# Performance work log

Hardware: AMD Instinct MI355X
Metric: run time of the kernel (lower is better)

## Reference

```python
import jax, jax.numpy as jnp
import numpy as np

D_MODEL, D_FF, D_KEY, D_VALUE, NUM_HEADS = 1024, 4096, 64, 64, 16
EPS = 1e-5
B, S = 2, 2048


def layer_norm(x, gamma, beta):
    # torch x.var() default is unbiased (ddof=1)
    mean = jnp.mean(x, axis=-1, keepdims=True)
    var = jnp.var(x, axis=-1, keepdims=True, ddof=1)
    return (x - mean) / jnp.sqrt(var + EPS) * gamma + beta


def setup_inputs() -> dict:
    key = jax.random.key(0)
    ks = jax.random.split(key, 16)
    s = 0.02
    return {
        "x": jax.random.normal(ks[0], (B, S, D_MODEL), dtype=jnp.float32),
        "mask": jnp.zeros((B, 1, 1, S), dtype=bool),
        "Wq": jax.random.normal(ks[1], (D_MODEL, NUM_HEADS * D_KEY), dtype=jnp.float32) * s,
        "bq": jnp.zeros((NUM_HEADS * D_KEY,), jnp.float32),
        "Wk": jax.random.normal(ks[2], (D_MODEL, NUM_HEADS * D_KEY), dtype=jnp.float32) * s,
        "bk": jnp.zeros((NUM_HEADS * D_KEY,), jnp.float32),
        "Wv": jax.random.normal(ks[3], (D_MODEL, NUM_HEADS * D_VALUE), dtype=jnp.float32) * s,
        "bv": jnp.zeros((NUM_HEADS * D_VALUE,), jnp.float32),
        "Wo": jax.random.normal(ks[4], (NUM_HEADS * D_VALUE, D_MODEL), dtype=jnp.float32) * s,
        "bo": jnp.zeros((D_MODEL,), jnp.float32),
        "gamma1": jnp.ones((D_MODEL,), jnp.float32),
        "beta1": jnp.zeros((D_MODEL,), jnp.float32),
        "W1": jax.random.normal(ks[5], (D_MODEL, D_FF), dtype=jnp.float32) * s,
        "b1": jnp.zeros((D_FF,), jnp.float32),
        "W2": jax.random.normal(ks[6], (D_FF, D_MODEL), dtype=jnp.float32) * s,
        "b2": jnp.zeros((D_MODEL,), jnp.float32),
        "gamma2": jnp.ones((D_MODEL,), jnp.float32),
        "beta2": jnp.zeros((D_MODEL,), jnp.float32),
    }


def reference(x, mask, Wq, bq, Wk, bk, Wv, bv, Wo, bo, gamma1, beta1, W1, b1, W2, b2, gamma2, beta2):
    Bsz, Sq, _ = x.shape
    # ---- multi-head attention (self-attention) ----
    q = (x @ Wq + bq).reshape(Bsz, Sq, NUM_HEADS, D_KEY)
    k = (x @ Wk + bk).reshape(Bsz, Sq, NUM_HEADS, D_KEY)
    v = (x @ Wv + bv).reshape(Bsz, Sq, NUM_HEADS, D_VALUE)
    scores = jnp.einsum("bqhd,bkhd->bhqk", q, k) / jnp.sqrt(jnp.float32(D_KEY))
    scores = jnp.where(mask, -jnp.inf, scores)
    attn = jax.nn.softmax(scores, axis=-1)
    ctx = jnp.einsum("bhqk,bkhd->bqhd", attn, v).reshape(Bsz, Sq, NUM_HEADS * D_VALUE)
    attn_out = ctx @ Wo + bo
    # ---- residual + LN, FFN, residual + LN ----
    h = layer_norm(attn_out + x, gamma1, beta1)
    ff = jnp.maximum(h @ W1 + b1, 0.0) @ W2 + b2
    out = layer_norm(ff + h, gamma2, beta2)
    return out
```

## Files before the change

kernel.cpp:

```cpp
#include <hip/hip_runtime.h>
#include <cstddef>
#include <cstdint>

#define BATCH   2
#define SEQ     2048
#define DMODEL  1024
#define DFF     4096
#define NHEADS  16
#define DHEAD   64
#define NTOK    (BATCH * SEQ)
#define LN_EPS  1e-5f

typedef __attribute__((ext_vector_type(8))) short bf16x8;
typedef __attribute__((ext_vector_type(4))) float f32x4;

#define MFMA(a, b, c) __builtin_amdgcn_mfma_f32_16x16x32_bf16((a), (b), (c), 0, 0, 0)

__device__ __forceinline__ unsigned short f2bf(float f) {
    unsigned int u = __float_as_uint(f);
    u += 0x7fffu + ((u >> 16) & 1u);
    return (unsigned short)(u >> 16);
}

__device__ __forceinline__ void gld_lds16(const void* g, void* l) {
    __builtin_amdgcn_global_load_lds(
        (const __attribute__((address_space(1))) void*)g,
        (__attribute__((address_space(3))) void*)l, 16, 0, 0);
}

template <int NT, bool RELU, bool RES, bool OUTBF16>
__global__ __launch_bounds__(256) void gemm_bt(
    const short* __restrict__ A, const short* __restrict__ Bt,
    const float* __restrict__ bias, const float* __restrict__ res,
    void* __restrict__ Cout, int M, int N, int K)
{
    constexpr int MI = (NT == 128) ? 4 : 2;
    __shared__ __align__(16) short As[128][32];
    __shared__ __align__(16) short Bs[NT][32];

    const int tid  = threadIdx.x;
    const int lane = tid & 63;
    const int w    = tid >> 6;
    const int row0 = blockIdx.y * 128;
    const int col0 = blockIdx.x * NT;
    const int wr   = (NT == 128) ? (w >> 1) * 64 : w * 32;
    const int wc   = (NT == 128) ? (w & 1) * 64 : 0;
    const int m    = lane & 15;
    const int q    = lane >> 4;

    f32x4 acc[MI][4] = {};

    const int sra = w * 32;
    const short* ga = A + (size_t)(row0 + sra + (lane >> 2)) * K + (lane & 3) * 8;
    short* lA0 = &As[sra][0];
    short* lA1 = &As[sra + 16][0];
    const int srb = (NT == 128) ? w * 32 : w * 16;
    const short* gb = Bt + (size_t)(col0 + srb + (lane >> 2)) * K + (lane & 3) * 8;
    short* lB0 = &Bs[srb][0];
    short* lB1 = (NT == 128) ? &Bs[srb + 16][0] : nullptr;

    for (int k0 = 0; k0 < K; k0 += 32) {
        gld_lds16(ga + k0, lA0);
        gld_lds16(ga + (size_t)16 * K + k0, lA1);
        gld_lds16(gb + k0, lB0);
        if (NT == 128) gld_lds16(gb + (size_t)16 * K + k0, lB1);
        __syncthreads();

        bf16x8 af[MI], bfr[4];
#pragma unroll
        for (int i = 0; i < MI; ++i) af[i]  = *(const bf16x8*)&As[wr + i * 16 + m][q * 8];
#pragma unroll
        for (int i = 0; i < 4; ++i)  bfr[i] = *(const bf16x8*)&Bs[wc + i * 16 + m][q * 8];
#pragma unroll
        for (int mi = 0; mi < MI; ++mi)
#pragma unroll
            for (int ni = 0; ni < 4; ++ni)
                acc[mi][ni] = MFMA(af[mi], bfr[ni], acc[mi][ni]);
        __syncthreads();
    }

#pragma unroll
    for (int mi = 0; mi < MI; ++mi) {
#pragma unroll
        for (int ni = 0; ni < 4; ++ni) {
            const int col = col0 + wc + ni * 16 + m;
            const float bv = bias[col];
#pragma unroll
            for (int r = 0; r < 4; ++r) {
                const int row = row0 + wr + mi * 16 + q * 4 + r;
                float v = acc[mi][ni][r] + bv;
                if (RES)  v += res[(size_t)row * N + col];
                if (RELU) v = fmaxf(v, 0.0f);
                if (OUTBF16)
                    ((unsigned short*)Cout)[(size_t)row * N + col] = f2bf(v);
                else
                    ((float*)Cout)[(size_t)row * N + col] = v;
            }
        }
    }
}

__global__ __launch_bounds__(256) void gemm_qkv(
    const short* __restrict__ A, const short* __restrict__ Bt,
    const float* __restrict__ bias, short* __restrict__ QKb,
    unsigned short* __restrict__ Vt)
{
    const int K = DMODEL;
    __shared__ __align__(16) short As[128][32];
    __shared__ __align__(16) short Bs[128][32];

    const int tid  = threadIdx.x;
    const int lane = tid & 63;
    const int w    = tid >> 6;
    const int row0 = blockIdx.y * 128;
    const int col0 = blockIdx.x * 128;
    const int wr   = (w >> 1) * 64;
    const int wc   = (w & 1) * 64;
    const int m    = lane & 15;
    const int q    = lane >> 4;

    f32x4 acc[4][4] = {};

    const int sr = w * 32;
    const short* ga = A  + (size_t)(row0 + sr + (lane >> 2)) * K + (lane & 3) * 8;
    const short* gb = Bt + (size_t)(col0 + sr + (lane >> 2)) * K + (lane & 3) * 8;
    short* lA0 = &As[sr][0];
    short* lA1 = &As[sr + 16][0];
    short* lB0 = &Bs[sr][0];
    short* lB1 = &Bs[sr + 16][0];

    for (int k0 = 0; k0 < K; k0 += 32) {
        gld_lds16(ga + k0, lA0);
        gld_lds16(ga + (size_t)16 * K + k0, lA1);
        gld_lds16(gb + k0, lB0);
        gld_lds16(gb + (size_t)16 * K + k0, lB1);
        __syncthreads();
        bf16x8 af[4], bfr[4];
#pragma unroll
        for (int i = 0; i < 4; ++i) af[i]  = *(const bf16x8*)&As[wr + i * 16 + m][q * 8];
#pragma unroll
        for (int i = 0; i < 4; ++i) bfr[i] = *(const bf16x8*)&Bs[wc + i * 16 + m][q * 8];
#pragma unroll
        for (int mi = 0; mi < 4; ++mi)
#pragma unroll
            for (int ni = 0; ni < 4; ++ni)
                acc[mi][ni] = MFMA(af[mi], bfr[ni], acc[mi][ni]);
        __syncthreads();
    }

    const int mode = (col0 >= 2048) ? 2 : (col0 < 1024 ? 0 : 1);
    const float scale = (mode == 0) ? 0.125f : 1.0f;
#pragma unroll
    for (int mi = 0; mi < 4; ++mi) {
#pragma unroll
        for (int ni = 0; ni < 4; ++ni) {
            const int col = col0 + wc + ni * 16 + m;
            const float bv = bias[col];
#pragma unroll
            for (int r = 0; r < 4; ++r) {
                const int row = row0 + wr + mi * 16 + q * 4 + r;
                const float v = (acc[mi][ni][r] + bv) * scale;
                if (mode < 2) {
                    QKb[(size_t)row * 2048 + col] = (short)f2bf(v);
                } else {
                    const int hd  = col - 2048;
                    const int bb  = row >> 11;
                    const int key = row & (SEQ - 1);
                    Vt[((size_t)(bb * 1024 + hd)) * SEQ + key] = f2bf(v);
                }
            }
        }
    }
}

__global__ __launch_bounds__(256) void attn_mfma(
    const short* __restrict__ Qp,
    const short* __restrict__ Kp,
    const short* __restrict__ Vtg,
    unsigned short* __restrict__ CTX)
{
    __shared__ __align__(16) short Ks[2][64][64];
    __shared__ __align__(16) short Vs[2][64][64];
    __shared__ __align__(16) short Ps[4][16][64];

    const int tid  = threadIdx.x;
    const int lane = tid & 63;
    const int w    = tid >> 6;
    const int b    = blockIdx.z;
    const int h    = blockIdx.y;
    const int q0   = blockIdx.x * 64;
    const int m    = lane & 15;
    const int qd   = lane >> 4;

    const short* gq = Qp + (size_t)(b * SEQ + q0 + w * 16 + m) * 2048 + h * 64;
    bf16x8 qreg[2];
    qreg[0] = *(const bf16x8*)(gq + qd * 8);
    qreg[1] = *(const bf16x8*)(gq + (qd + 4) * 8);

    const int cg = (lane & 7) ^ (lane >> 3);
    const short* Kg = Kp  + (size_t)(b * SEQ) * 2048 + h * 64 + cg * 8;
    const short* Vg = Vtg + (size_t)(b * 1024 + h * 64) * SEQ + cg * 8;

    {
        const short* gk = Kg + (size_t)(w * 16 + (lane >> 3)) * 2048;
        gld_lds16(gk,            &Ks[0][w * 16][0]);
        gld_lds16(gk + 8 * 2048, &Ks[0][w * 16 + 8][0]);
        const short* gv = Vg + (size_t)(w * 16 + (lane >> 3)) * SEQ;
        gld_lds16(gv,            &Vs[0][w * 16][0]);
        gld_lds16(gv + 8 * SEQ,  &Vs[0][w * 16 + 8][0]);
    }

    float lrow[4] = {0.f, 0.f, 0.f, 0.f};
    f32x4 oacc[4] = {};

    for (int j = 0; j < SEQ / 64; ++j) {
        const int cur = j & 1;
        __syncthreads();
        if (j + 1 < SEQ / 64) {
            const int nb = 1 - cur;
            const short* gk = Kg + (size_t)((j + 1) * 64 + w * 16 + (lane >> 3)) * 2048;
            gld_lds16(gk,            &Ks[nb][w * 16][0]);
            gld_lds16(gk + 8 * 2048, &Ks[nb][w * 16 + 8][0]);
            const short* gv = Vg + (size_t)(w * 16 + (lane >> 3)) * SEQ + (j + 1) * 64;
            gld_lds16(gv,            &Vs[nb][w * 16][0]);
            gld_lds16(gv + 8 * SEQ,  &Vs[nb][w * 16 + 8][0]);
        }

        f32x4 sacc[4] = {};
#pragma unroll
        for (int ks = 0; ks < 2; ++ks) {
            const int kc = ks * 4 + qd;
#pragma unroll
            for (int ni = 0; ni < 4; ++ni) {
                const int kn = ni * 16 + m;
                bf16x8 bk = *(const bf16x8*)&Ks[cur][kn][(kc ^ (kn & 7)) * 8];
                sacc[ni] = MFMA(qreg[ks], bk, sacc[ni]);
            }
        }

        float rsum[4] = {0.f, 0.f, 0.f, 0.f};
#pragma unroll
        for (int ni = 0; ni < 4; ++ni)
#pragma unroll
            for (int r = 0; r < 4; ++r) {
                const float p = __expf(sacc[ni][r]);
                sacc[ni][r] = p;
                rsum[r] += p;
            }
#pragma unroll
        for (int off = 1; off < 16; off <<= 1)
#pragma unroll
            for (int r = 0; r < 4; ++r) rsum[r] += __shfl_xor(rsum[r], off, 64);
#pragma unroll
        for (int r = 0; r < 4; ++r) lrow[r] += rsum[r];

#pragma unroll
        for (int ni = 0; ni < 4; ++ni)
#pragma unroll
            for (int r = 0; r < 4; ++r) {
                const int row = qd * 4 + r;
                const int swc = (ni * 2 + (m >> 3)) ^ (row & 7);
                Ps[w][row][swc * 8 + (m & 7)] = (short)f2bf(sacc[ni][r]);
            }

#pragma unroll
        for (int ks = 0; ks < 2; ++ks) {
            const int kc = ks * 4 + qd;
            bf16x8 ap = *(const bf16x8*)&Ps[w][m][(kc ^ (m & 7)) * 8];
#pragma unroll
            for (int ni = 0; ni < 4; ++ni) {
                const int dn = ni * 16 + m;
                bf16x8 bv = *(const bf16x8*)&Vs[cur][dn][(kc ^ (dn & 7)) * 8];
                oacc[ni] = MFMA(ap, bv, oacc[ni]);
            }
        }
    }

    float inv[4];
#pragma unroll
    for (int r = 0; r < 4; ++r) inv[r] = 1.0f / lrow[r];
#pragma unroll
    for (int ni = 0; ni < 4; ++ni)
#pragma unroll
        for (int r = 0; r < 4; ++r) {
            const int row = q0 + w * 16 + qd * 4 + r;
            const int col = h * 64 + ni * 16 + m;
            CTX[(size_t)(b * SEQ + row) * DMODEL + col] = f2bf(oacc[ni][r] * inv[r]);
        }
}

__global__ __launch_bounds__(256) void wtrans(
    const float* __restrict__ W, short* __restrict__ Wt, int K, int N)
{
    __shared__ float t[32][33];
    const int tid = threadIdx.x;
    const int c = tid & 31, r8 = tid >> 5;
    const int bx = blockIdx.x * 32, by = blockIdx.y * 32;
#pragma unroll
    for (int i = 0; i < 4; ++i)
        t[r8 + i * 8][c] = W[(size_t)(by + r8 + i * 8) * N + bx + c];
    __syncthreads();
#pragma unroll
    for (int i = 0; i < 4; ++i)
        Wt[(size_t)(bx + r8 + i * 8) * K + by + c] = (short)f2bf(t[c][r8 + i * 8]);
}

__global__ __launch_bounds__(256) void xconv(
    const float* __restrict__ X, short* __restrict__ Y)
{
    const size_t i = ((size_t)blockIdx.x * 256 + threadIdx.x) * 4;
    const float4 v = *(const float4*)(X + i);
    short4 o;
    o.x = (short)f2bf(v.x); o.y = (short)f2bf(v.y);
    o.z = (short)f2bf(v.z); o.w = (short)f2bf(v.w);
    *(short4*)(Y + i) = o;
}

__global__ __launch_bounds__(256) void packb(
    const float* __restrict__ bq, const float* __restrict__ bk,
    const float* __restrict__ bv, float* __restrict__ bqkv)
{
    const int i = blockIdx.x * 256 + threadIdx.x;
    const float v = (i < 1024) ? bq[i] : (i < 2048 ? bk[i - 1024] : bv[i - 2048]);
    bqkv[i] = v;
}

template <bool BF16OUT>
__global__ __launch_bounds__(256) void ln_kernel(
    const float* __restrict__ X, const float* __restrict__ gamma,
    const float* __restrict__ beta, float* __restrict__ Y,
    short* __restrict__ Yb)
{
    const int row = blockIdx.x;
    const int tid = threadIdx.x;
    __shared__ float red[256];

    const float4 xv = ((const float4*)(X + (size_t)row * DMODEL))[tid];

    red[tid] = xv.x + xv.y + xv.z + xv.w;
    __syncthreads();
    for (int st = 128; st > 0; st >>= 1) {
        if (tid < st) red[tid] += red[tid + st];
        __syncthreads();
    }
    const float mean = red[0] / (float)DMODEL;
    __syncthreads();

    const float dx0 = xv.x - mean, dx1 = xv.y - mean;
    const float dx2 = xv.z - mean, dx3 = xv.w - mean;
    red[tid] = dx0 * dx0 + dx1 * dx1 + dx2 * dx2 + dx3 * dx3;
    __syncthreads();
    for (int st = 128; st > 0; st >>= 1) {
        if (tid < st) red[tid] += red[tid + st];
        __syncthreads();
    }
    const float var = red[0] / (float)(DMODEL - 1);
    const float rs = rsqrtf(var + LN_EPS);

    const float4 gv = ((const float4*)gamma)[tid];
    const float4 bv = ((const float4*)beta)[tid];
    float4 o;
    o.x = dx0 * rs * gv.x + bv.x;
    o.y = dx1 * rs * gv.y + bv.y;
    o.z = dx2 * rs * gv.z + bv.z;
    o.w = dx3 * rs * gv.w + bv.w;
    ((float4*)(Y + (size_t)row * DMODEL))[tid] = o;
    if (BF16OUT) {
        short4 ob;
        ob.x = (short)f2bf(o.x); ob.y = (short)f2bf(o.y);
        ob.z = (short)f2bf(o.z); ob.w = (short)f2bf(o.w);
        *(short4*)(Yb + (size_t)row * DMODEL + tid * 4) = ob;
    }
}

extern "C" void kernel_launch(void* const* d_in, const int* in_sizes, int n_in,
                              void* d_out, int out_size, void* d_ws, size_t ws_size,
                              hipStream_t stream)
{
    const float* x   = (const float*)d_in[0];
    const float* Wq  = (const float*)d_in[2];
    const float* bq  = (const float*)d_in[3];
    const float* Wk  = (const float*)d_in[4];
    const float* bk  = (const float*)d_in[5];
    const float* Wv  = (const float*)d_in[6];
    const float* bv  = (const float*)d_in[7];
    const float* Wo  = (const float*)d_in[8];
    const float* bo  = (const float*)d_in[9];
    const float* g1  = (const float*)d_in[10];
    const float* be1 = (const float*)d_in[11];
    const float* W1  = (const float*)d_in[12];
    const float* b1  = (const float*)d_in[13];
    const float* W2  = (const float*)d_in[14];
    const float* b2  = (const float*)d_in[15];
    const float* g2  = (const float*)d_in[16];
    const float* be2 = (const float*)d_in[17];
    float* out = (float*)d_out;
    char*  ws  = (char*)d_ws;
    (void)in_sizes; (void)n_in; (void)out_size; (void)ws_size;

    const size_t MB = 1ull << 20;
    short* xb    = (short*)(ws);
    short* W1t   = (short*)(ws + 8 * MB);
    short* W2t   = (short*)(ws + 16 * MB);
    short* Wqkvt = (short*)(ws + 24 * MB);
    short* Wot   = (short*)(ws + 30 * MB);
    float* bqkv  = (float*)(ws + 32 * MB);
    short* QKb   = (short*)(ws + 33 * MB);
    unsigned short* Vtg = (unsigned short*)(ws + 49 * MB);
    unsigned short* CTX = (unsigned short*)(ws + 57 * MB);
    float* A1    = (float*)(ws + 33 * MB);
    short* Hb    = (short*)(ws);
    short* F1    = (short*)(ws + 49 * MB);

    dim3 blk(256);

    xconv<<<dim3(NTOK * DMODEL / 1024), blk, 0, stream>>>(x, xb);
    packb<<<dim3(12), blk, 0, stream>>>(bq, bk, bv, bqkv);
    wtrans<<<dim3(32, 32), blk, 0, stream>>>(Wq, Wqkvt, DMODEL, DMODEL);
    wtrans<<<dim3(32, 32), blk, 0, stream>>>(Wk, Wqkvt + 1024 * 1024, DMODEL, DMODEL);
    wtrans<<<dim3(32, 32), blk, 0, stream>>>(Wv, Wqkvt + 2048 * 1024, DMODEL, DMODEL);
    wtrans<<<dim3(32, 32), blk, 0, stream>>>(Wo, Wot, DMODEL, DMODEL);
    wtrans<<<dim3(DFF / 32, DMODEL / 32), blk, 0, stream>>>(W1, W1t, DMODEL, DFF);
    wtrans<<<dim3(DMODEL / 32, DFF / 32), blk, 0, stream>>>(W2, W2t, DFF, DMODEL);

    gemm_qkv<<<dim3(3072 / 128, NTOK / 128), blk, 0, stream>>>(xb, Wqkvt, bqkv, QKb, Vtg);

    attn_mfma<<<dim3(SEQ / 64, NHEADS, BATCH), blk, 0, stream>>>(
        QKb, QKb + 1024, (const short*)Vtg, CTX);

    gemm_bt<64, false, true, false><<<dim3(1024 / 64, NTOK / 128), blk, 0, stream>>>(
        (const short*)CTX, Wot, bo, x, A1, NTOK, DMODEL, DMODEL);
    ln_kernel<true><<<NTOK, blk, 0, stream>>>(A1, g1, be1, A1, Hb);

    gemm_bt<128, true, false, true><<<dim3(DFF / 128, NTOK / 128), blk, 0, stream>>>(
        Hb, W1t, b1, nullptr, F1, NTOK, DFF, DMODEL);
    gemm_bt<64, false, true, false><<<dim3(1024 / 64, NTOK / 128), blk, 0, stream>>>(
        F1, W2t, b2, A1, out, NTOK, DMODEL, DFF);
    ln_kernel<false><<<NTOK, blk, 0, stream>>>(out, g2, be2, out, nullptr);
}
```

Measured before the change: 433.2 us.

## Add K=64 swizzled GEMM, MFMA row sums in attention, batch weight transposes

Adds a gemm_bt64 kernel for the N=1024 output GEMMs (Wo and W2). It uses a K-step of 64 with XOR-swizzled LDS, which halves the barrier count per K and avoids bank conflicts. In attention, the per-row softmax sum now comes from an extra MFMA against a ones vector instead of shuffle reductions, and P is truncated to bf16 rather than rounded. The four 1024x1024 weight transposes are merged into one launch. Truncation slightly changes numerics, and the new sum accumulates the bf16-rounded P values rather than the fp32 ones.

```diff
diff --git a/kernel.cpp b/kernel.cpp
--- a/kernel.cpp
+++ b/kernel.cpp
@@ -28,51 +28,49 @@
         (__attribute__((address_space(3))) void*)l, 16, 0, 0);
 }
 
-template <int NT, bool RELU, bool RES, bool OUTBF16>
+template <bool RELU, bool RES, bool OUTBF16>
 __global__ __launch_bounds__(256) void gemm_bt(
     const short* __restrict__ A, const short* __restrict__ Bt,
     const float* __restrict__ bias, const float* __restrict__ res,
     void* __restrict__ Cout, int M, int N, int K)
 {
-    constexpr int MI = (NT == 128) ? 4 : 2;
     __shared__ __align__(16) short As[128][32];
-    __shared__ __align__(16) short Bs[NT][32];
+    __shared__ __align__(16) short Bs[128][32];
 
     const int tid  = threadIdx.x;
     const int lane = tid & 63;
     const int w    = tid >> 6;
     const int row0 = blockIdx.y * 128;
-    const int col0 = blockIdx.x * NT;
-    const int wr   = (NT == 128) ? (w >> 1) * 64 : w * 32;
-    const int wc   = (NT == 128) ? (w & 1) * 64 : 0;
+    const int col0 = blockIdx.x * 128;
+    const int wr   = (w >> 1) * 64;
+    const int wc   = (w & 1) * 64;
     const int m    = lane & 15;
     const int q    = lane >> 4;
 
-    f32x4 acc[MI][4] = {};
-
-    const int sra = w * 32;
-    const short* ga = A + (size_t)(row0 + sra + (lane >> 2)) * K + (lane & 3) * 8;
-    short* lA0 = &As[sra][0];
-    short* lA1 = &As[sra + 16][0];
-    const int srb = (NT == 128) ? w * 32 : w * 16;
-    const short* gb = Bt + (size_t)(col0 + srb + (lane >> 2)) * K + (lane & 3) * 8;
-    short* lB0 = &Bs[srb][0];
-    short* lB1 = (NT == 128) ? &Bs[srb + 16][0] : nullptr;
+    f32x4 acc[4][4] = {};
+
+    const int sr = w * 32;
+    const short* ga = A  + (size_t)(row0 + sr + (lane >> 2)) * K + (lane & 3) * 8;
+    const short* gb = Bt + (size_t)(col0 + sr + (lane >> 2)) * K + (lane & 3) * 8;
+    short* lA0 = &As[sr][0];
+    short* lA1 = &As[sr + 16][0];
+    short* lB0 = &Bs[sr][0];
+    short* lB1 = &Bs[sr + 16][0];
 
     for (int k0 = 0; k0 < K; k0 += 32) {
         gld_lds16(ga + k0, lA0);
         gld_lds16(ga + (size_t)16 * K + k0, lA1);
         gld_lds16(gb + k0, lB0);
-        if (NT == 128) gld_lds16(gb + (size_t)16 * K + k0, lB1);
-        __syncthreads();
-
-        bf16x8 af[MI], bfr[4];
-#pragma unroll
-        for (int i = 0; i < MI; ++i) af[i]  = *(const bf16x8*)&As[wr + i * 16 + m][q * 8];
-#pragma unroll
-        for (int i = 0; i < 4; ++i)  bfr[i] = *(const bf16x8*)&Bs[wc + i * 16 + m][q * 8];
-#pragma unroll
-        for (int mi = 0; mi < MI; ++mi)
+        gld_lds16(gb + (size_t)16 * K + k0, lB1);
+        __syncthreads();
+
+        bf16x8 af[4], bfr[4];
+#pragma unroll
+        for (int i = 0; i < 4; ++i) af[i]  = *(const bf16x8*)&As[wr + i * 16 + m][q * 8];
+#pragma unroll
+        for (int i = 0; i < 4; ++i) bfr[i] = *(const bf16x8*)&Bs[wc + i * 16 + m][q * 8];
+#pragma unroll
+        for (int mi = 0; mi < 4; ++mi)
 #pragma unroll
             for (int ni = 0; ni < 4; ++ni)
                 acc[mi][ni] = MFMA(af[mi], bfr[ni], acc[mi][ni]);
@@ -80,10 +78,86 @@
     }
 
 #pragma unroll
-    for (int mi = 0; mi < MI; ++mi) {
+    for (int mi = 0; mi < 4; ++mi) {
 #pragma unroll
         for (int ni = 0; ni < 4; ++ni) {
             const int col = col0 + wc + ni * 16 + m;
+            const float bv = bias[col];
+#pragma unroll
+            for (int r = 0; r < 4; ++r) {
+                const int row = row0 + wr + mi * 16 + q * 4 + r;
+                float v = acc[mi][ni][r] + bv;
+                if (RES)  v += res[(size_t)row * N + col];
+                if (RELU) v = fmaxf(v, 0.0f);
+                if (OUTBF16)
+                    ((unsigned short*)Cout)[(size_t)row * N + col] = f2bf(v);
+                else
+                    ((float*)Cout)[(size_t)row * N + col] = v;
+            }
+        }
+    }
+}
+
+template <bool RELU, bool RES, bool OUTBF16>
+__global__ __launch_bounds__(256) void gemm_bt64(
+    const short* __restrict__ A, const short* __restrict__ Bt,
+    const float* __restrict__ bias, const float* __restrict__ res,
+    void* __restrict__ Cout, int M, int N, int K)
+{
+    __shared__ __align__(16) short As[128][64];
+    __shared__ __align__(16) short Bs[64][64];
+
+    const int tid  = threadIdx.x;
+    const int lane = tid & 63;
+    const int w    = tid >> 6;
+    const int row0 = blockIdx.y * 128;
+    const int col0 = blockIdx.x * 64;
+    const int wr   = w * 32;
+    const int m    = lane & 15;
+    const int q    = lane >> 4;
+
+    f32x4 acc[2][4] = {};
+
+    const int cg = (lane & 7) ^ ((lane >> 3) & 7);
+    const short* ga = A + (size_t)(row0 + w * 32 + (lane >> 3)) * K + cg * 8;
+    const short* gb = Bt + (size_t)(col0 + w * 16 + (lane >> 3)) * K + cg * 8;
+
+    for (int k0 = 0; k0 < K; k0 += 64) {
+#pragma unroll
+        for (int i = 0; i < 4; ++i)
+            gld_lds16(ga + (size_t)i * 8 * K + k0, &As[w * 32 + i * 8][0]);
+#pragma unroll
+        for (int i = 0; i < 2; ++i)
+            gld_lds16(gb + (size_t)i * 8 * K + k0, &Bs[w * 16 + i * 8][0]);
+        __syncthreads();
+
+#pragma unroll
+        for (int kk = 0; kk < 2; ++kk) {
+            bf16x8 af[2], bfr[4];
+#pragma unroll
+            for (int i = 0; i < 2; ++i) {
+                const int row = wr + i * 16 + m;
+                af[i] = *(const bf16x8*)&As[row][((kk * 4 + q) ^ (row & 7)) * 8];
+            }
+#pragma unroll
+            for (int i = 0; i < 4; ++i) {
+                const int row = i * 16 + m;
+                bfr[i] = *(const bf16x8*)&Bs[row][((kk * 4 + q) ^ (row & 7)) * 8];
+            }
+#pragma unroll
+            for (int mi = 0; mi < 2; ++mi)
+#pragma unroll
+                for (int ni = 0; ni < 4; ++ni)
+                    acc[mi][ni] = MFMA(af[mi], bfr[ni], acc[mi][ni]);
+        }
+        __syncthreads();
+    }
+
+#pragma unroll
+    for (int mi = 0; mi < 2; ++mi) {
+#pragma unroll
+        for (int ni = 0; ni < 4; ++ni) {
+            const int col = col0 + ni * 16 + m;
             const float bv = bias[col];
 #pragma unroll
             for (int r = 0; r < 4; ++r) {
@@ -197,6 +271,10 @@
     qreg[0] = *(const bf16x8*)(gq + qd * 8);
     qreg[1] = *(const bf16x8*)(gq + (qd + 4) * 8);
 
+    bf16x8 bones;
+#pragma unroll
+    for (int c = 0; c < 8; ++c) bones[c] = (short)0x3F80;
+
     const int cg = (lane & 7) ^ (lane >> 3);
     const short* Kg = Kp  + (size_t)(b * SEQ) * 2048 + h * 64 + cg * 8;
     const short* Vg = Vtg + (size_t)(b * 1024 + h * 64) * SEQ + cg * 8;
@@ -210,7 +288,7 @@
         gld_lds16(gv + 8 * SEQ,  &Vs[0][w * 16 + 8][0]);
     }
 
-    float lrow[4] = {0.f, 0.f, 0.f, 0.f};
+    f32x4 lacc = {};
     f32x4 oacc[4] = {};
 
     for (int j = 0; j < SEQ / 64; ++j) {
@@ -238,35 +316,21 @@
             }
         }
 
-        float rsum[4] = {0.f, 0.f, 0.f, 0.f};
 #pragma unroll
         for (int ni = 0; ni < 4; ++ni)
 #pragma unroll
             for (int r = 0; r < 4; ++r) {
                 const float p = __expf(sacc[ni][r]);
-                sacc[ni][r] = p;
-                rsum[r] += p;
-            }
-#pragma unroll
-        for (int off = 1; off < 16; off <<= 1)
-#pragma unroll
-            for (int r = 0; r < 4; ++r) rsum[r] += __shfl_xor(rsum[r], off, 64);
-#pragma unroll
-        for (int r = 0; r < 4; ++r) lrow[r] += rsum[r];
-
-#pragma unroll
-        for (int ni = 0; ni < 4; ++ni)
-#pragma unroll
-            for (int r = 0; r < 4; ++r) {
                 const int row = qd * 4 + r;
                 const int swc = (ni * 2 + (m >> 3)) ^ (row & 7);
-                Ps[w][row][swc * 8 + (m & 7)] = (short)f2bf(sacc[ni][r]);
+                Ps[w][row][swc * 8 + (m & 7)] = (short)(__float_as_uint(p) >> 16);
             }
 
 #pragma unroll
         for (int ks = 0; ks < 2; ++ks) {
             const int kc = ks * 4 + qd;
             bf16x8 ap = *(const bf16x8*)&Ps[w][m][(kc ^ (m & 7)) * 8];
+            lacc = MFMA(ap, bones, lacc);
 #pragma unroll
             for (int ni = 0; ni < 4; ++ni) {
                 const int dn = ni * 16 + m;
@@ -278,7 +342,7 @@
 
     float inv[4];
 #pragma unroll
-    for (int r = 0; r < 4; ++r) inv[r] = 1.0f / lrow[r];
+    for (int r = 0; r < 4; ++r) inv[r] = 1.0f / lacc[r];
 #pragma unroll
     for (int ni = 0; ni < 4; ++ni)
 #pragma unroll
@@ -303,6 +367,27 @@
 #pragma unroll
     for (int i = 0; i < 4; ++i)
         Wt[(size_t)(bx + r8 + i * 8) * K + by + c] = (short)f2bf(t[c][r8 + i * 8]);
+}
+
+__global__ __launch_bounds__(256) void wtrans4(
+    const float* __restrict__ Wa, const float* __restrict__ Wb,
+    const float* __restrict__ Wc, const float* __restrict__ Wd,
+    short* __restrict__ Dqkv, short* __restrict__ Do)
+{
+    __shared__ float t[32][33];
+    const float* W = (blockIdx.z == 0) ? Wa : (blockIdx.z == 1) ? Wb
+                   : (blockIdx.z == 2) ? Wc : Wd;
+    short* Wt = (blockIdx.z == 3) ? Do : (Dqkv + (size_t)blockIdx.z * 1024 * 1024);
+    const int tid = threadIdx.x;
+    const int c = tid & 31, r8 = tid >> 5;
+    const int bx = blockIdx.x * 32, by = blockIdx.y * 32;
+#pragma unroll
+    for (int i = 0; i < 4; ++i)
+        t[r8 + i * 8][c] = W[(size_t)(by + r8 + i * 8) * 1024 + bx + c];
+    __syncthreads();
+#pragma unroll
+    for (int i = 0; i < 4; ++i)
+        Wt[(size_t)(bx + r8 + i * 8) * 1024 + by + c] = (short)f2bf(t[c][r8 + i * 8]);
 }
 
 __global__ __launch_bounds__(256) void xconv(
@@ -416,10 +501,7 @@
 
     xconv<<<dim3(NTOK * DMODEL / 1024), blk, 0, stream>>>(x, xb);
     packb<<<dim3(12), blk, 0, stream>>>(bq, bk, bv, bqkv);
-    wtrans<<<dim3(32, 32), blk, 0, stream>>>(Wq, Wqkvt, DMODEL, DMODEL);
-    wtrans<<<dim3(32, 32), blk, 0, stream>>>(Wk, Wqkvt + 1024 * 1024, DMODEL, DMODEL);
-    wtrans<<<dim3(32, 32), blk, 0, stream>>>(Wv, Wqkvt + 2048 * 1024, DMODEL, DMODEL);
-    wtrans<<<dim3(32, 32), blk, 0, stream>>>(Wo, Wot, DMODEL, DMODEL);
+    wtrans4<<<dim3(32, 32, 4), blk, 0, stream>>>(Wq, Wk, Wv, Wo, Wqkvt, Wot);
     wtrans<<<dim3(DFF / 32, DMODEL / 32), blk, 0, stream>>>(W1, W1t, DMODEL, DFF);
     wtrans<<<dim3(DMODEL / 32, DFF / 32), blk, 0, stream>>>(W2, W2t, DFF, DMODEL);
 
@@ -428,13 +510,13 @@
     attn_mfma<<<dim3(SEQ / 64, NHEADS, BATCH), blk, 0, stream>>>(
         QKb, QKb + 1024, (const short*)Vtg, CTX);
 
-    gemm_bt<64, false, true, false><<<dim3(1024 / 64, NTOK / 128), blk, 0, stream>>>(
+    gemm_bt64<false, true, false><<<dim3(1024 / 64, NTOK / 128), blk, 0, stream>>>(
         (const short*)CTX, Wot, bo, x, A1, NTOK, DMODEL, DMODEL);
     ln_kernel<true><<<NTOK, blk, 0, stream>>>(A1, g1, be1, A1, Hb);
 
-    gemm_bt<128, true, false, true><<<dim3(DFF / 128, NTOK / 128), blk, 0, stream>>>(
+    gemm_bt<true, false, true><<<dim3(DFF / 128, NTOK / 128), blk, 0, stream>>>(
         Hb, W1t, b1, nullptr, F1, NTOK, DFF, DMODEL);
-    gemm_bt<64, false, true, false><<<dim3(1024 / 64, NTOK / 128), blk, 0, stream>>>(
+    gemm_bt64<false, true, false><<<dim3(1024 / 64, NTOK / 128), blk, 0, stream>>>(
         F1, W2t, b2, A1, out, NTOK, DMODEL, DFF);
     ln_kernel<false><<<NTOK, blk, 0, stream>>>(out, g2, be2, out, nullptr);
 }
```

Result: faster. 394.4 us (-9.0%).
